# Kernel optimization log

Measured on AMD Instinct MI355X. Metric: run time of the kernel, lower is better.

Reference implementation:

```python
import jax, jax.numpy as jnp
import numpy as np

N_HEADS = 12


def setup_inputs() -> dict:
    key = jax.random.key(0)
    ks = jax.random.split(key, 4)
    B, S, D = 2, 2048, 768
    x = jax.random.normal(ks[0], (B, S, D), dtype=jnp.float32)
    # nn.Linear-style init scale ~ 1/sqrt(D) to keep logits reasonable
    scale = 1.0 / np.sqrt(D)
    Wq = jax.random.normal(ks[1], (D, D), dtype=jnp.float32) * scale
    Wk = jax.random.normal(ks[2], (D, D), dtype=jnp.float32) * scale
    Wv = jax.random.normal(ks[3], (D, D), dtype=jnp.float32) * scale
    bq = jnp.zeros((D,), jnp.float32)
    bk = jnp.zeros((D,), jnp.float32)
    bv = jnp.zeros((D,), jnp.float32)
    mask = jnp.ones((B, S), jnp.int32)
    return {"x": x, "Wq": Wq, "bq": bq, "Wk": Wk, "bk": bk,
            "Wv": Wv, "bv": bv, "mask": mask}


def reference(x, Wq, bq, Wk, bk, Wv, bv, mask):
    B, S, D = x.shape
    H = N_HEADS
    W = D // H
    # q,k,v: (B,S,D) -> (B,H,S,W)
    def proj(Wm, bm):
        return (x @ Wm.T + bm).reshape(B, S, H, W).transpose(0, 2, 1, 3)
    q, k, v = proj(Wq, bq), proj(Wk, bk), proj(Wv, bv)
    scores = jnp.einsum("bhsw,bhtw->bhst", q, k) / jnp.sqrt(
        jnp.asarray(W, x.dtype))
    # mask: (B,S) -> broadcast over query positions; 0 -> -1e20
    scores = jnp.where(mask[:, None, None, :] == 0,
                       jnp.asarray(-1e20, scores.dtype), scores)
    attn = jax.nn.softmax(scores, axis=-1)  # (B,H,S,S)
    # dropout p=0.0 (eval) -> identity
    ctx = jnp.einsum("bhst,bhtw->bhsw", attn, v)
    hidden = ctx.transpose(0, 2, 1, 3).reshape(B, S, D)
    return hidden
```

## Files before the change

kernel.cpp:

```cpp
#include <hip/hip_runtime.h>
#include <hip/hip_bf16.h>
#include <stdint.h>


typedef __attribute__((ext_vector_type(8))) short bf16x8;
typedef __attribute__((ext_vector_type(4))) float f32x4;
typedef __attribute__((ext_vector_type(16))) float f32x16;
typedef __attribute__((ext_vector_type(8))) unsigned short u16x8;

#define MFMA16(a, b, c) __builtin_amdgcn_mfma_f32_16x16x32_bf16((a), (b), (c), 0, 0, 0)
#define MFMA32(a, b, c) __builtin_amdgcn_mfma_f32_32x32x16_bf16((a), (b), (c), 0, 0, 0)
#define SWZ(row, colb) ((colb) ^ (((row) & 7) << 4))

union U32x4BF {
  unsigned u[4];
  bf16x8 v;
};

__device__ __forceinline__ void gl_lds16(const void* g, void* l) {
  __builtin_amdgcn_global_load_lds(
      (__attribute__((address_space(1))) void*)const_cast<void*>(g),
      (__attribute__((address_space(3))) void*)l, 16, 0, 0);
}

__device__ __forceinline__ unsigned short f2bf(float x) {
  unsigned int v = __float_as_uint(x);
  return (unsigned short)((v + 0x7fffu + ((v >> 16) & 1u)) >> 16);
}

__global__ __launch_bounds__(256) void cvt_all(
    const float* __restrict__ x, const float* __restrict__ wq,
    const float* __restrict__ wk, const float* __restrict__ wv,
    unsigned short* __restrict__ xb, unsigned short* __restrict__ wb) {
  int i = blockIdx.x * 256 + threadIdx.x;
  const float* s;
  unsigned short* d;
  int off;
  if (i < 393216)      { s = x;  d = xb;            off = i; }
  else if (i < 466944) { s = wq; d = wb;            off = i - 393216; }
  else if (i < 540672) { s = wk; d = wb + 589824;   off = i - 466944; }
  else                 { s = wv; d = wb + 1179648;  off = i - 540672; }
  const float4* sp = (const float4*)s + (size_t)off * 2;
  float4 a = sp[0], b2 = sp[1];
  u16x8 o;
  o[0] = f2bf(a.x); o[1] = f2bf(a.y); o[2] = f2bf(a.z); o[3] = f2bf(a.w);
  o[4] = f2bf(b2.x); o[5] = f2bf(b2.y); o[6] = f2bf(b2.z); o[7] = f2bf(b2.w);
  *((u16x8*)d + off) = o;
}

__global__ __launch_bounds__(256) void proj_gemm(
    const unsigned short* __restrict__ xb, const unsigned short* __restrict__ wb,
    const float* __restrict__ bq, const float* __restrict__ bk, const float* __restrict__ bv,
    unsigned short* __restrict__ qw, unsigned short* __restrict__ kx,
    unsigned short* __restrict__ vx) {
  __shared__ __align__(16) char psmem[49152];
  const int t = threadIdx.x, lane = t & 63, wave = t >> 6;
  const int lo = lane & 15, hi = lane >> 4;
  const int wr = wave >> 1, wc = wave & 1;
  const int mbase = blockIdx.x * 128;
  const int wsel = blockIdx.y / 6;
  const int nbase = (blockIdx.y % 6) * 128;
  const char* xc = (const char*)xb;
  const char* wmc = (const char*)(wb + (size_t)wsel * 589824);

  const int pp0 = t * 16, pp1 = t * 16 + 4096;
  const int ar0 = pp0 >> 7, ac0 = (pp0 & 127) ^ ((ar0 & 7) << 4);
  const int am0 = ((ac0 >> 6) << 6) + ar0, ak0 = ac0 & 63;
  const int ar1 = pp1 >> 7, ac1 = (pp1 & 127) ^ ((ar1 & 7) << 4);
  const int am1 = ((ac1 >> 6) << 6) + ar1, ak1 = ac1 & 63;

  const char* xa0 = xc + (size_t)(mbase + am0) * 1536 + ak0;
  const char* xa1 = xc + (size_t)(mbase + am1) * 1536 + ak1;
  const char* wa0 = wmc + (size_t)(nbase + am0) * 1536 + ak0;
  const char* wa1 = wmc + (size_t)(nbase + am1) * 1536 + ak1;

#define PSTAGE(BUF)                              \
  do {                                           \
    char* lb = psmem + (BUF) * 16384;            \
    gl_lds16(xa0, lb + pp0);                     \
    gl_lds16(xa1, lb + pp1);                     \
    gl_lds16(wa0, lb + 8192 + pp0);              \
    gl_lds16(wa1, lb + 8192 + pp1);              \
    xa0 += 64; xa1 += 64; wa0 += 64; wa1 += 64;  \
  } while (0)

  f32x4 acc[4][4];
#pragma unroll
  for (int i = 0; i < 4; i++)
#pragma unroll
    for (int j = 0; j < 4; j++) acc[i][j] = (f32x4){0.f, 0.f, 0.f, 0.f};

  const int axor = (lo & 7) << 4;
  PSTAGE(0);
  PSTAGE(1);
  int cur = 0, sb = 2;
#pragma unroll 1
  for (int it = 0; it < 24; ++it) {
    if (it < 22) {
      PSTAGE(sb);
      asm volatile("s_waitcnt vmcnt(8)" ::: "memory");
    } else if (it == 22) {
      asm volatile("s_waitcnt vmcnt(4)" ::: "memory");
    } else {
      asm volatile("s_waitcnt vmcnt(0)" ::: "memory");
    }
    __builtin_amdgcn_s_barrier();
    const char* lA = psmem + cur * 16384;
    const char* lB = lA + 8192;

    bf16x8 af[4], bf[4];
#pragma unroll
    for (int mf = 0; mf < 4; mf++)
      af[mf] = *(const bf16x8*)(lA + (mf * 16 + lo) * 128 + ((wr * 64 + hi * 16) ^ axor));
#pragma unroll
    for (int nf = 0; nf < 4; nf++)
      bf[nf] = *(const bf16x8*)(lB + (nf * 16 + lo) * 128 + ((wc * 64 + hi * 16) ^ axor));

    __builtin_amdgcn_s_setprio(1);
    if (wsel == 2) {
#pragma unroll
      for (int mf = 0; mf < 4; mf++)
#pragma unroll
        for (int nf = 0; nf < 4; nf++) acc[mf][nf] = MFMA16(bf[nf], af[mf], acc[mf][nf]);
    } else {
#pragma unroll
      for (int mf = 0; mf < 4; mf++)
#pragma unroll
        for (int nf = 0; nf < 4; nf++) acc[mf][nf] = MFMA16(af[mf], bf[nf], acc[mf][nf]);
    }
    __builtin_amdgcn_s_setprio(0);
    __builtin_amdgcn_s_barrier();
    cur = (cur == 2) ? 0 : cur + 1;
    sb = (sb == 2) ? 0 : sb + 1;
  }
#undef PSTAGE

  const float QSCALE = 0.125f * 1.44269504089f;
  if (wsel == 2) {
#pragma unroll
    for (int nf = 0; nf < 4; nf++) {
#pragma unroll
      for (int mf = 0; mf < 4; mf++) {
#pragma unroll
        for (int r = 0; r < 4; r++) {
          int n = nbase + wc * 64 + nf * 16 + hi * 4 + r;
          int m = mbase + wr * 64 + mf * 16 + lo;
          int b_ = m >> 11, s = m & 2047;
          int h = n >> 6, w = n & 63;
          float val = acc[mf][nf][r] + bv[n];
          size_t bhh = (size_t)b_ * 12 + h;
          size_t idx = bhh * 131072 + (size_t)(s >> 5) * 2048 + (size_t)((w >> 5) & 1) * 1024 +
                       (size_t)((s >> 4) & 1) * 512 +
                       (size_t)((w & 31) + 32 * ((s >> 3) & 1)) * 8 + (s & 7);
          vx[idx] = f2bf(val);
        }
      }
    }
  } else {
    const float* bias = (wsel == 0) ? bq : bk;
#pragma unroll
    for (int nf = 0; nf < 4; nf++) {
      int n = nbase + wc * 64 + nf * 16 + lo;
      float bv_ = bias[n];
      int h = n >> 6, wcol = n & 63;
#pragma unroll
      for (int mf = 0; mf < 4; mf++) {
#pragma unroll
        for (int r = 0; r < 4; r++) {
          int m = mbase + wr * 64 + mf * 16 + hi * 4 + r;
          int b_ = m >> 11, s = m & 2047;
          float val = acc[mf][nf][r] + bv_;
          size_t bhh = (size_t)b_ * 12 + h;
          if (wsel == 0) {
            qw[(bhh * 2048 + s) * 64 + wcol] = f2bf(val * QSCALE);
          } else {
            int d = wcol;
            size_t idx = bhh * 131072 + (size_t)(s >> 5) * 2048 + (size_t)(d >> 4) * 512 +
                         (size_t)((s & 31) + 32 * ((d >> 3) & 1)) * 8 + (d & 7);
            kx[idx] = f2bf(val);
          }
        }
      }
    }
  }
}

__global__ __launch_bounds__(256) void attn_kernel(
    const unsigned short* __restrict__ qw, const unsigned short* __restrict__ kx,
    const unsigned short* __restrict__ vx, const int* __restrict__ mask,
    float* __restrict__ out) {
  __shared__ __align__(16) char smem[17152];
  const int t = threadIdx.x, lane = t & 63, wave = t >> 6;
  const int wq = wave >> 1, wk = wave & 1;
  const int l31 = lane & 31, hl = lane >> 5;
  const int qb = blockIdx.x, bh = blockIdx.y;
  const int b = bh / 12, hh = bh - b * 12;

  {
    const int* mb = mask + (size_t)b * 2048 + t * 8;
    int4 a0 = *(const int4*)mb;
    int4 a1 = *(const int4*)(mb + 4);
    unsigned by = (unsigned)(a0.x != 0) | ((unsigned)(a0.y != 0) << 1) |
                  ((unsigned)(a0.z != 0) << 2) | ((unsigned)(a0.w != 0) << 3) |
                  ((unsigned)(a1.x != 0) << 4) | ((unsigned)(a1.y != 0) << 5) |
                  ((unsigned)(a1.z != 0) << 6) | ((unsigned)(a1.w != 0) << 7);
    smem[16384 + t] = (char)by;
  }
  __syncthreads();
  const unsigned balv = *(const unsigned*)(smem + 16384 + (wk * 32 + l31) * 4);

  bf16x8 qv[4];
  {
    int qrow = qb * 64 + wq * 32 + l31;
    const char* qp = (const char*)qw + ((size_t)bh * 2048 + qrow) * 128 + hl * 16;
#pragma unroll
    for (int s = 0; s < 4; s++) qv[s] = *(const bf16x8*)(qp + s * 32);
  }

  const char* kp = (const char*)kx + (size_t)bh * 262144 + (size_t)wk * 131072 + lane * 16;
  const char* vp = (const char*)vx + (size_t)bh * 262144 + (size_t)wk * 131072 + lane * 16;

  f32x16 oacc[2];
#pragma unroll
  for (int wh = 0; wh < 2; wh++)
#pragma unroll
    for (int g = 0; g < 16; g++) oacc[wh][g] = 0.f;
  float lacc = 0.f;

  bf16x8 ka0 = *(const bf16x8*)(kp);
  bf16x8 ka1 = *(const bf16x8*)(kp + 1024);
  bf16x8 ka2 = *(const bf16x8*)(kp + 2048);
  bf16x8 ka3 = *(const bf16x8*)(kp + 3072);
  kp += 4096;

#pragma unroll 2
  for (int it = 0; it < 32; ++it) {
    bf16x8 v00 = *(const bf16x8*)(vp);
    bf16x8 v01 = *(const bf16x8*)(vp + 1024);
    bf16x8 v10 = *(const bf16x8*)(vp + 2048);
    bf16x8 v11 = *(const bf16x8*)(vp + 3072);
    vp += 4096;

    f32x16 sc;
#pragma unroll
    for (int g = 0; g < 16; g++) sc[g] = 0.f;
    __builtin_amdgcn_s_setprio(1);
    sc = MFMA32(ka0, qv[0], sc);
    sc = MFMA32(ka1, qv[1], sc);
    sc = MFMA32(ka2, qv[2], sc);
    sc = MFMA32(ka3, qv[3], sc);
    __builtin_amdgcn_s_setprio(0);

    ka0 = *(const bf16x8*)(kp);
    ka1 = *(const bf16x8*)(kp + 1024);
    ka2 = *(const bf16x8*)(kp + 2048);
    ka3 = *(const bf16x8*)(kp + 3072);
    kp += 4096;

    unsigned bal = __builtin_amdgcn_readlane(balv, it);
    if (bal != 0xFFFFFFFFu) {
#pragma unroll
      for (int g = 0; g < 16; g++) {
        int key = (g & 3) + 8 * (g >> 2) + 4 * hl;
        if (!((bal >> key) & 1)) sc[g] = -30000.f;
      }
    }

#pragma unroll
    for (int g = 0; g < 16; g++) {
      float e_;
      asm("v_exp_f32 %0, %1" : "=v"(e_) : "v"(sc[g]));
      sc[g] = e_;
    }
    lacc += (((sc[0] + sc[1]) + (sc[2] + sc[3])) + ((sc[4] + sc[5]) + (sc[6] + sc[7]))) +
            (((sc[8] + sc[9]) + (sc[10] + sc[11])) + ((sc[12] + sc[13]) + (sc[14] + sc[15])));
    unsigned pk[4][2];
#pragma unroll
    for (int m = 0; m < 4; m++) {
      asm("v_cvt_pk_bf16_f32 %0, %1, %2" : "=v"(pk[m][0]) : "v"(sc[4 * m]), "v"(sc[4 * m + 1]));
      asm("v_cvt_pk_bf16_f32 %0, %1, %2" : "=v"(pk[m][1]) : "v"(sc[4 * m + 2]), "v"(sc[4 * m + 3]));
    }
    U32x4BF apv[2];
#pragma unroll
    for (int sp = 0; sp < 2; sp++)
#pragma unroll
      for (int cp = 0; cp < 2; cp++) {
        unsigned xx = pk[2 * sp][cp], yy = pk[2 * sp + 1][cp];
        asm("v_permlane32_swap_b32 %0, %1" : "+v"(xx), "+v"(yy));
        apv[sp].u[cp] = xx;
        apv[sp].u[2 + cp] = yy;
      }

    __builtin_amdgcn_s_setprio(1);
    oacc[0] = MFMA32(apv[0].v, v00, oacc[0]);
    oacc[0] = MFMA32(apv[1].v, v01, oacc[0]);
    oacc[1] = MFMA32(apv[0].v, v10, oacc[1]);
    oacc[1] = MFMA32(apv[1].v, v11, oacc[1]);
    __builtin_amdgcn_s_setprio(0);
  }

  lacc += __shfl_xor(lacc, 32);
  if (lane < 32)
    *(float*)(smem + 16640 + (((wq * 32 + l31) << 1) + wk) * 4) = lacc;
  if (wk == 1) {
#pragma unroll
    for (int wh = 0; wh < 2; wh++) {
      int vrow = wh * 32 + l31;
#pragma unroll
      for (int m = 0; m < 4; m++) {
        f32x4 part = (f32x4){oacc[wh][4 * m], oacc[wh][4 * m + 1],
                             oacc[wh][4 * m + 2], oacc[wh][4 * m + 3]};
        *(f32x4*)(smem + wq * 8192 + vrow * 128 + SWZ(vrow, hl * 16 + m * 32)) = part;
      }
    }
  }
  __syncthreads();
  if (wk == 0) {
    float linv[16];
#pragma unroll
    for (int g = 0; g < 16; g++) {
      int qrow = 4 * hl + (g & 3) + 8 * (g >> 2);
      float2 lp = *(const float2*)(smem + 16640 + ((wq * 32 + qrow) << 3));
      linv[g] = __builtin_amdgcn_rcpf(lp.x + lp.y);
    }
#pragma unroll
    for (int wh = 0; wh < 2; wh++) {
      int vrow = wh * 32 + l31;
#pragma unroll
      for (int m = 0; m < 4; m++) {
        f32x4 part = *(const f32x4*)(smem + wq * 8192 + vrow * 128 + SWZ(vrow, hl * 16 + m * 32));
#pragma unroll
        for (int r = 0; r < 4; r++) {
          int g = 4 * m + r;
          int qrow = 4 * hl + r + 8 * m;
          float val = (oacc[wh][g] + part[r]) * linv[g];
          out[((size_t)b * 2048 + qb * 64 + wq * 32 + qrow) * 768 + hh * 64 + wh * 32 + l31] =
              val;
        }
      }
    }
  }
}

extern "C" void kernel_launch(void* const* d_in, const int* in_sizes, int n_in,
                              void* d_out, int out_size, void* d_ws, size_t ws_size,
                              hipStream_t stream) {
  (void)in_sizes; (void)n_in; (void)out_size; (void)ws_size;
  const float* x  = (const float*)d_in[0];
  const float* Wq = (const float*)d_in[1];
  const float* bq = (const float*)d_in[2];
  const float* Wk = (const float*)d_in[3];
  const float* bk = (const float*)d_in[4];
  const float* Wv = (const float*)d_in[5];
  const float* bv = (const float*)d_in[6];
  const int* mask = (const int*)d_in[7];
  float* out = (float*)d_out;

  char* ws = (char*)d_ws;
  unsigned short* xb = (unsigned short*)(ws);
  unsigned short* wb = (unsigned short*)(ws + 6291456);
  unsigned short* qw = (unsigned short*)(ws + 9830400);
  unsigned short* kx = (unsigned short*)(ws + 16121856);
  unsigned short* vx = (unsigned short*)(ws + 22413312);

  cvt_all<<<2400, 256, 0, stream>>>(x, Wq, Wk, Wv, xb, wb);
  proj_gemm<<<dim3(32, 18), 256, 0, stream>>>(xb, wb, bq, bk, bv, qw, kx, vx);
  attn_kernel<<<dim3(32, 24), 256, 0, stream>>>(qw, kx, vx, mask, out);
}
```

Measured before the change: 93.18 us.

## Write K/V in plain layouts from GEMM and relayout via separate LDS kernel

```diff
diff --git a/kernel.cpp b/kernel.cpp
--- a/kernel.cpp
+++ b/kernel.cpp
@@ -51,8 +51,8 @@
 __global__ __launch_bounds__(256) void proj_gemm(
     const unsigned short* __restrict__ xb, const unsigned short* __restrict__ wb,
     const float* __restrict__ bq, const float* __restrict__ bk, const float* __restrict__ bv,
-    unsigned short* __restrict__ qw, unsigned short* __restrict__ kx,
-    unsigned short* __restrict__ vx) {
+    unsigned short* __restrict__ qw, unsigned short* __restrict__ kw,
+    unsigned short* __restrict__ vw) {
   __shared__ __align__(16) char psmem[49152];
   const int t = threadIdx.x, lane = t & 63, wave = t >> 6;
   const int lo = lane & 15, hi = lane >> 4;
@@ -146,13 +146,9 @@
           int n = nbase + wc * 64 + nf * 16 + hi * 4 + r;
           int m = mbase + wr * 64 + mf * 16 + lo;
           int b_ = m >> 11, s = m & 2047;
-          int h = n >> 6, w = n & 63;
+          int h = n >> 6, wcol = n & 63;
           float val = acc[mf][nf][r] + bv[n];
-          size_t bhh = (size_t)b_ * 12 + h;
-          size_t idx = bhh * 131072 + (size_t)(s >> 5) * 2048 + (size_t)((w >> 5) & 1) * 1024 +
-                       (size_t)((s >> 4) & 1) * 512 +
-                       (size_t)((w & 31) + 32 * ((s >> 3) & 1)) * 8 + (s & 7);
-          vx[idx] = f2bf(val);
+          vw[(((size_t)b_ * 12 + h) * 64 + wcol) * 2048 + s] = f2bf(val);
         }
       }
     }
@@ -171,17 +167,53 @@
           int b_ = m >> 11, s = m & 2047;
           float val = acc[mf][nf][r] + bv_;
           size_t bhh = (size_t)b_ * 12 + h;
-          if (wsel == 0) {
+          if (wsel == 0)
             qw[(bhh * 2048 + s) * 64 + wcol] = f2bf(val * QSCALE);
-          } else {
-            int d = wcol;
-            size_t idx = bhh * 131072 + (size_t)(s >> 5) * 2048 + (size_t)(d >> 4) * 512 +
-                         (size_t)((s & 31) + 32 * ((d >> 3) & 1)) * 8 + (d & 7);
-            kx[idx] = f2bf(val);
-          }
+          else
+            kw[(bhh * 2048 + s) * 64 + wcol] = f2bf(val);
         }
       }
     }
+  }
+}
+
+__global__ __launch_bounds__(256) void relayout_kv(
+    const unsigned short* kw, const unsigned short* __restrict__ vwT,
+    unsigned short* __restrict__ kx, unsigned short* vx) {
+  __shared__ __align__(16) char rsm[32768];
+  const int t = threadIdx.x;
+  const int ktq = blockIdx.x, bh = blockIdx.y;
+  const size_t bhb = (size_t)bh * 262144;
+  const int kt0 = ktq * 4;
+
+  {
+    const int key = t >> 3;
+    const int d0 = (t & 7) * 8;
+    const char* ksrc = (const char*)kw + bhb + (size_t)kt0 * 4096 + key * 128 + d0 * 2;
+    char* kldst = rsm + (d0 >> 4) * 1024 + ((d0 >> 3) & 1) * 512 + key * 16;
+#pragma unroll
+    for (int c = 0; c < 4; c++)
+      *(u16x8*)(kldst + c * 4096) = *(const u16x8*)(ksrc + c * 4096);
+  }
+  {
+    const int w = t >> 2;
+    const int sl0 = (t & 3) * 8;
+    const char* vsrc = (const char*)vwT + bhb + (size_t)w * 4096 + (kt0 * 32 + sl0) * 2;
+    char* vldst = rsm + 16384 + (w >> 5) * 2048 + ((sl0 >> 4) & 1) * 1024 +
+                  ((sl0 >> 3) & 1) * 512 + (w & 31) * 16;
+#pragma unroll
+    for (int c = 0; c < 4; c++)
+      *(u16x8*)(vldst + c * 4096) = *(const u16x8*)(vsrc + c * 64);
+  }
+  __syncthreads();
+
+  char* kdst = (char*)kx + bhb + (size_t)ktq * 16384;
+  char* vdst = (char*)vx + bhb + (size_t)ktq * 16384;
+#pragma unroll
+  for (int c = 0; c < 4; c++) {
+    int lb = c * 4096 + t * 16;
+    *(u16x8*)(kdst + lb) = *(const u16x8*)(rsm + lb);
+    *(u16x8*)(vdst + lb) = *(const u16x8*)(rsm + 16384 + lb);
   }
 }
 
@@ -357,13 +389,16 @@
   float* out = (float*)d_out;
 
   char* ws = (char*)d_ws;
-  unsigned short* xb = (unsigned short*)(ws);
-  unsigned short* wb = (unsigned short*)(ws + 6291456);
-  unsigned short* qw = (unsigned short*)(ws + 9830400);
-  unsigned short* kx = (unsigned short*)(ws + 16121856);
-  unsigned short* vx = (unsigned short*)(ws + 22413312);
+  unsigned short* xb  = (unsigned short*)(ws);
+  unsigned short* wb  = (unsigned short*)(ws + 6291456);
+  unsigned short* qw  = (unsigned short*)(ws + 9830400);
+  unsigned short* kw  = (unsigned short*)(ws + 16121856);
+  unsigned short* vwT = (unsigned short*)(ws + 22413312);
+  unsigned short* kx  = (unsigned short*)(ws);
+  unsigned short* vx  = (unsigned short*)(ws + 16121856);
 
   cvt_all<<<2400, 256, 0, stream>>>(x, Wq, Wk, Wv, xb, wb);
-  proj_gemm<<<dim3(32, 18), 256, 0, stream>>>(xb, wb, bq, bk, bv, qw, kx, vx);
+  proj_gemm<<<dim3(32, 18), 256, 0, stream>>>(xb, wb, bq, bk, bv, qw, kw, vwT);
+  relayout_kv<<<dim3(16, 24), 256, 0, stream>>>(kw, vwT, kx, vx);
   attn_kernel<<<dim3(32, 24), 256, 0, stream>>>(qw, kx, vx, mask, out);
 }
```

Result: faster. 85.92 us (-7.8%).
